# Optimization experiments

Measured on AMD Instinct MI355X. Metric: run time of the kernel, lower is better.

Reference implementation:

```python
import jax, jax.numpy as jnp
import numpy as np

HEADS = 8

def _grid_edges(H, W):
    # 4-neighbor grid adjacency, built at trace time (static), faithful to the torch double loop
    N = H * W
    idx = np.arange(N).reshape(H, W)
    e = np.zeros((N, N), np.float32)
    a, b = idx[1:, :].ravel(), idx[:-1, :].ravel()
    e[a, b] = 1.0; e[b, a] = 1.0
    a, b = idx[:, 1:].ravel(), idx[:, :-1].ravel()
    e[a, b] = 1.0; e[b, a] = 1.0
    return jnp.asarray(e)

def _layernorm(x, g, b, eps=1e-5):
    m = x.mean(-1, keepdims=True)
    v = x.var(-1, keepdims=True)
    return (x - m) / jnp.sqrt(v + eps) * g + b

def _gat(nodes, edges, W, b, rel):
    # nodes: [N,B,E]; W: [4,E,E] (q,k,v,out); rel: [HEADS]
    N, B, E = nodes.shape
    hd = E // HEADS
    q = (nodes @ W[0].T + b[0]).reshape(N, B, HEADS, hd)
    k = (nodes @ W[1].T + b[1]).reshape(N, B, HEADS, hd)
    v = (nodes @ W[2].T + b[2]).reshape(N, B, HEADS, hd)
    s = jnp.einsum('ibhd,jbhd->hbij', q, k) / float(np.sqrt(hd))
    s = s + edges[None, None] * rel[:, None, None, None]  # per-head edge relation bias
    a = jax.nn.softmax(s, axis=1)  # faithful to source: softmax over dim=1 (batch axis)
    o = jnp.einsum('hbij,jbhd->ibhd', a, v).reshape(N, B, E)
    return o @ W[3].T + b[3]

def _mha(q_in, kv_in, W, b):
    # standard nn.MultiheadAttention (eval, no dropout); seq-first [L,B,E]
    L, B, E = q_in.shape
    S = kv_in.shape[0]
    hd = E // HEADS
    q = (q_in @ W[0].T + b[0]).reshape(L, B, HEADS, hd)
    k = (kv_in @ W[1].T + b[1]).reshape(S, B, HEADS, hd)
    v = (kv_in @ W[2].T + b[2]).reshape(S, B, HEADS, hd)
    s = jnp.einsum('ibhd,jbhd->hbij', q, k) / float(np.sqrt(hd))
    a = jax.nn.softmax(s, axis=-1)
    o = jnp.einsum('hbij,jbhd->ibhd', a, v).reshape(L, B, E)
    return o @ W[3].T + b[3]

def reference(x, gat_W, gat_b, gat_rel, cross_W, cross_b, ln_g, ln_b):
    B, C, H, W = x.shape
    P = H // 4
    # global nodes: avg_pool2d(kernel=4) then flatten to [P*P, B, C]
    g = x.reshape(B, C, P, 4, P, 4).mean(axis=(3, 5))
    global_nodes = g.reshape(B, C, P * P).transpose(2, 0, 1)
    global_edges = jnp.ones((P * P, P * P), x.dtype)
    local_nodes = x.reshape(B, C, H * W).transpose(2, 0, 1)  # [HW,B,C]
    local_edges = _grid_edges(H, W)
    g_out = _gat(global_nodes, global_edges, gat_W[0], gat_b[0], gat_rel[0])
    g_out = _layernorm(g_out + global_nodes, ln_g[0], ln_b[0])
    l_out = _gat(local_nodes, local_edges, gat_W[1], gat_b[1], gat_rel[1])
    l_out = _layernorm(l_out + local_nodes, ln_g[1], ln_b[1])
    # nearest upsample x4 of global output back to HxW
    g_map = g_out.transpose(1, 2, 0).reshape(B, C, P, P)
    g_up = jnp.repeat(jnp.repeat(g_map, 4, axis=2), 4, axis=3)
    g_up = g_up.reshape(B, C, H * W).transpose(2, 0, 1)
    c_out = _mha(l_out, g_up, cross_W, cross_b)
    c_out = _layernorm(c_out + l_out, ln_g[2], ln_b[2])
    return c_out.transpose(1, 2, 0).reshape(B, C, H, W)

def setup_inputs() -> dict:
    key = jax.random.key(0)
    ks = jax.random.split(key, 6)
    B, C, H, W = 2, 256, 40, 40
    E = C
    sc = 0.02
    return {
        "x": jax.random.normal(ks[0], (B, C, H, W), jnp.float32),
        "gat_W": jax.random.normal(ks[1], (2, 4, E, E), jnp.float32) * sc,
        "gat_b": jax.random.normal(ks[2], (2, 4, E), jnp.float32) * sc,
        "gat_rel": jax.random.normal(ks[3], (2, HEADS), jnp.float32),
        "cross_W": jax.random.normal(ks[4], (4, E, E), jnp.float32) * sc,
        "cross_b": jax.random.normal(ks[5], (4, E), jnp.float32) * sc,
        "ln_g": jnp.ones((3, E), jnp.float32),
        "ln_b": jnp.zeros((3, E), jnp.float32),
    }
```

## Files before the change

### kernel.cpp

```cpp
#include <hip/hip_runtime.h>
#include <math.h>

#define NLOC 1600
#define NGLO 100

typedef unsigned short u16;
typedef short s16x8 __attribute__((ext_vector_type(8)));
typedef float f32x4 __attribute__((ext_vector_type(4)));

__device__ __forceinline__ short f2bf(float f) {
    unsigned u = __float_as_uint(f);
    u += 0x7fffu + ((u >> 16) & 1u);
    return (short)(u >> 16);
}
__device__ __forceinline__ float bf2f(u16 h) {
    return __uint_as_float(((unsigned)h) << 16);
}


__device__ __forceinline__ void gemm_tile(int lane, const u16* __restrict__ A,
                                          const u16* __restrict__ W,
                                          const float* __restrict__ bias,
                                          u16* __restrict__ C, int M, int m0, int n0) {
    int c = lane & 15, qd = lane >> 4;
    f32x4 acc[2][4] = {};
#pragma unroll 2
    for (int kc = 0; kc < 8; ++kc) {
        int ko = kc * 32 + qd * 8;
        s16x8 af[2], bf[4];
#pragma unroll
        for (int mi = 0; mi < 2; ++mi) {
            int row = m0 + mi * 16 + c;
            s16x8 zz = {};
            af[mi] = (row < M) ? *(const s16x8*)(A + (size_t)row * 256 + ko) : zz;
        }
#pragma unroll
        for (int ni = 0; ni < 4; ++ni)
            bf[ni] = *(const s16x8*)(W + (size_t)(n0 + ni * 16 + c) * 256 + ko);
#pragma unroll
        for (int mi = 0; mi < 2; ++mi)
#pragma unroll
            for (int ni = 0; ni < 4; ++ni)
                acc[mi][ni] = __builtin_amdgcn_mfma_f32_16x16x32_bf16(af[mi], bf[ni],
                                                                      acc[mi][ni], 0, 0, 0);
    }
#pragma unroll
    for (int mi = 0; mi < 2; ++mi)
#pragma unroll
        for (int r = 0; r < 4; ++r) {
            int row = m0 + mi * 16 + 4 * qd + r;
            if (row < M) {
#pragma unroll
                for (int ni = 0; ni < 4; ++ni) {
                    int col = n0 + ni * 16 + c;
                    C[(size_t)row * 256 + col] = (u16)f2bf(acc[mi][ni][r] + bias[col]);
                }
            }
        }
}

template <int MODE>
__device__ __forceinline__ void gemmln_block(int tid, const u16* __restrict__ A,
                                             const u16* __restrict__ W,
                                             const float* __restrict__ bias,
                                             const float* __restrict__ R,
                                             const float* __restrict__ g,
                                             const float* __restrict__ bb,
                                             float* fout, u16* bfout, float* dout,
                                             int M, int m0) {
    int w = tid >> 6, lane = tid & 63;
    int c = lane & 15, qd = lane >> 4;
    int n0 = w * 64;

    f32x4 acc[4] = {};
#pragma unroll 2
    for (int kc = 0; kc < 8; ++kc) {
        int ko = kc * 32 + qd * 8;
        int row = m0 + c;
        s16x8 zz = {};
        s16x8 af = (row < M) ? *(const s16x8*)(A + (size_t)row * 256 + ko) : zz;
#pragma unroll
        for (int ni = 0; ni < 4; ++ni) {
            s16x8 bf = *(const s16x8*)(W + (size_t)(n0 + ni * 16 + c) * 256 + ko);
            acc[ni] = __builtin_amdgcn_mfma_f32_16x16x32_bf16(af, bf, acc[ni], 0, 0, 0);
        }
    }

    __shared__ float ps1[4][16], ps2[4][16];
    float v[4][4];
#pragma unroll
    for (int r = 0; r < 4; ++r) {
        int row = m0 + 4 * qd + r;
        bool ok = (row < M);
        float s1 = 0.f, s2 = 0.f;
#pragma unroll
        for (int ni = 0; ni < 4; ++ni) {
            int col = n0 + ni * 16 + c;
            float val = acc[ni][r] + bias[col] + (ok ? R[(size_t)row * 256 + col] : 0.f);
            v[r][ni] = val;
            s1 += val; s2 += val * val;
        }
        s1 += __shfl_xor(s1, 1); s2 += __shfl_xor(s2, 1);
        s1 += __shfl_xor(s1, 2); s2 += __shfl_xor(s2, 2);
        s1 += __shfl_xor(s1, 4); s2 += __shfl_xor(s2, 4);
        s1 += __shfl_xor(s1, 8); s2 += __shfl_xor(s2, 8);
        if (c == 0) { ps1[w][4 * qd + r] = s1; ps2[w][4 * qd + r] = s2; }
    }
    __syncthreads();

    if (MODE == 0) {
#pragma unroll
        for (int r = 0; r < 4; ++r) {
            int lr = 4 * qd + r;
            int row = m0 + lr;
            if (row >= M) continue;
            float s1 = ps1[0][lr] + ps1[1][lr] + ps1[2][lr] + ps1[3][lr];
            float s2 = ps2[0][lr] + ps2[1][lr] + ps2[2][lr] + ps2[3][lr];
            float mean = s1 * (1.f / 256.f);
            float var  = s2 * (1.f / 256.f) - mean * mean;
            float rstd = rsqrtf(var + 1e-5f);
#pragma unroll
            for (int ni = 0; ni < 4; ++ni) {
                int col = n0 + ni * 16 + c;
                float y = (v[r][ni] - mean) * rstd * g[col] + bb[col];
                fout[(size_t)row * 256 + col] = y;
                bfout[(size_t)row * 256 + col] = (u16)f2bf(y);
            }
        }
    } else {
        __shared__ float ytile[2][8][256];
#pragma unroll
        for (int r = 0; r < 4; ++r) {
            int lr = 4 * qd + r;
            float s1 = ps1[0][lr] + ps1[1][lr] + ps1[2][lr] + ps1[3][lr];
            float s2 = ps2[0][lr] + ps2[1][lr] + ps2[2][lr] + ps2[3][lr];
            float mean = s1 * (1.f / 256.f);
            float var  = s2 * (1.f / 256.f) - mean * mean;
            float rstd = rsqrtf(var + 1e-5f);
#pragma unroll
            for (int ni = 0; ni < 4; ++ni) {
                int col = n0 + ni * 16 + c;
                ytile[lr & 1][lr >> 1][col] = (v[r][ni] - mean) * rstd * g[col] + bb[col];
            }
        }
        __syncthreads();
#pragma unroll
        for (int p = tid; p < 512; p += 256) {
            int b = p >> 8, col = p & 255;
            float4 y0, y1;
            y0.x = ytile[b][0][col]; y0.y = ytile[b][1][col];
            y0.z = ytile[b][2][col]; y0.w = ytile[b][3][col];
            y1.x = ytile[b][4][col]; y1.y = ytile[b][5][col];
            y1.z = ytile[b][6][col]; y1.w = ytile[b][7][col];
            size_t o = ((size_t)(b * 256 + col)) * 1600 + (m0 >> 1);
            *(float4*)(dout + o)     = y0;
            *(float4*)(dout + o + 4) = y1;
        }
    }
}

__global__ __launch_bounds__(256) void k_prep(const float* __restrict__ gw,
                                              const float* __restrict__ cw,
                                              u16* __restrict__ gwb,
                                              u16* __restrict__ cwb,
                                              const float* __restrict__ x,
                                              float* __restrict__ nodes,
                                              u16* __restrict__ nodesb,
                                              float* __restrict__ gn,
                                              u16* __restrict__ gnb) {
    int bx = blockIdx.x;
    if (bx < 768) {
        int t = bx * 256 + threadIdx.x;
        const float* src; u16* dst; int idx;
        if (t < 131072) { src = gw; dst = gwb; idx = t; }
        else            { src = cw; dst = cwb; idx = t - 131072; }
        float4 v = ((const float4*)src)[idx];
        ushort4 o;
        o.x = (u16)f2bf(v.x); o.y = (u16)f2bf(v.y);
        o.z = (u16)f2bf(v.z); o.w = (u16)f2bf(v.w);
        ((ushort4*)dst)[idx] = o;
        return;
    }
    int bid = bx - 768;
    if (bid < 3200) {
        int t = bid * 256 + threadIdx.x;
        int c = t & 255;
        int b = (t >> 8) & 1;
        int n = t >> 9;
        float v = x[((size_t)(b * 256 + c)) * 1600 + n];
        nodes[t] = v;
        nodesb[t] = (u16)f2bf(v);
    } else {
        int t = (bid - 3200) * 256 + threadIdx.x;
        int c = t & 255;
        int b = (t >> 8) & 1;
        int n = t >> 9;
        int p = n / 10, qq = n - p * 10;
        const float* xp = x + ((size_t)(b * 256 + c)) * 1600 + (p * 4) * 40 + qq * 4;
        float s = 0.f;
#pragma unroll
        for (int dy = 0; dy < 4; ++dy)
#pragma unroll
            for (int dx = 0; dx < 4; ++dx)
                s += xp[dy * 40 + dx];
        s *= (1.f / 16.f);
        gn[t] = s;
        gnb[t] = (u16)f2bf(s);
    }
}

__global__ __launch_bounds__(64) void k_qkv(const u16* __restrict__ nodesb,
                                            const u16* __restrict__ gnb,
                                            const u16* __restrict__ W1b,
                                            const u16* __restrict__ W0b,
                                            const float* __restrict__ b1,
                                            const float* __restrict__ b0,
                                            u16* __restrict__ qbuf,
                                            u16* __restrict__ gqb,
                                            float* __restrict__ sv1) {
    int lane = threadIdx.x;
    int bx = blockIdx.x, z = blockIdx.z;
    int n0 = blockIdx.y * 64;
    if (bx == 100 && blockIdx.y == 0 && z == 0) {
#pragma unroll
        for (int i = 0; i < 8; ++i) sv1[lane * 8 + i] = 0.f;
    }
    if (bx < 100)
        gemm_tile(lane, nodesb, W1b + (size_t)z * 65536, b1 + z * 256,
                  qbuf + (size_t)z * 819200, 3200, bx * 32, n0);
    else
        gemm_tile(lane, gnb, W0b + (size_t)z * 65536, b0 + z * 256,
                  gqb + (size_t)z * 51200, 200, (bx - 100) * 32, n0);
}

__device__ __forceinline__ void vtrans_block(const u16* __restrict__ src,
                                             u16* __restrict__ dst,
                                             int M, int Npad, int bxx, int byy,
                                             float* sum) {
    __shared__ u16 tile[32][33];
    int m0 = bxx * 32;
    int e0 = byy * 32;
    int tx = threadIdx.x & 31, ty = threadIdx.x >> 5;
#pragma unroll
    for (int k2 = 0; k2 < 4; ++k2) {
        int m = m0 + ty + k2 * 8;
        tile[ty + k2 * 8][tx] = (m < M) ? src[(size_t)m * 256 + e0 + tx] : (u16)0;
    }
    __syncthreads();
    int b = tx >> 4, nl = tx & 15;
    int n = (m0 >> 1) + nl;
    if (n < Npad) {
#pragma unroll
        for (int k2 = 0; k2 < 4; ++k2) {
            int e = e0 + ty + k2 * 8;
            dst[(size_t)(b * 256 + e) * Npad + n] = tile[2 * nl + b][ty + k2 * 8];
        }
    }
    if (threadIdx.x < 32) {
        float s = 0.f;
#pragma unroll
        for (int r = 0; r < 16; ++r) s += bf2f(tile[2 * r + 1][threadIdx.x]);
        atomicAdd(&sum[e0 + threadIdx.x], s);
    }
}

__global__ __launch_bounds__(256) void k_vtrans(const u16* __restrict__ vbuf,
                                                u16* __restrict__ vtb,
                                                const u16* __restrict__ gvb,
                                                u16* __restrict__ gvt,
                                                float* __restrict__ sv1l,
                                                float* __restrict__ sv1g) {
    int bx = blockIdx.x;
    if (bx < 100) vtrans_block(vbuf, vtb, 3200, 1600, bx, blockIdx.y, sv1l);
    else          vtrans_block(gvb, gvt, 200, 128, bx - 100, blockIdx.y, sv1g);
}

__global__ __launch_bounds__(256) void k_attn(
    const u16* __restrict__ qb, const u16* __restrict__ kb,
    const u16* __restrict__ vt, float* __restrict__ pO, float* __restrict__ pT,
    const u16* __restrict__ gqb, const u16* __restrict__ gkb,
    const u16* __restrict__ gvt, const float* __restrict__ sv1g,
    u16* __restrict__ gattb)
{
    __shared__ u16 ks[2][32][40];
    __shared__ u16 vs[2][32][40];
    __shared__ short At4[4][16][40];

    int tid = threadIdx.x;
    int w = tid >> 6, lane = tid & 63;
    int c = lane & 15, qd = lane >> 4;
    int bx = blockIdx.x;

    if (bx < 800) {
        int q4 = bx & 3;
        int hic = bx >> 2;
        int ic = hic % 25, h = hic / 25;
        int hb = h * 32;
        int i0 = ic * 64 + w * 16;
        int jb0 = q4 * 13, jbe = (jb0 + 13 < 50) ? jb0 + 13 : 50;

        const u16* qp = qb + ((size_t)(i0 + c) * 2) * 256 + hb + qd * 8;
        s16x8 qf0 = *(const s16x8*)qp;
        s16x8 qf1 = *(const s16x8*)(qp + 256);
#pragma unroll
        for (int z = 0; z < 8; ++z) qf0[z] ^= (short)0x8000;

        f32x4 o0[2] = {}, t1[2] = {};

        int srow = tid >> 2, part = tid & 3;
        int sjl = srow >> 1, sb = srow & 1;
        int vb_ = srow >> 5, vd = srow & 31;

        for (int jb = jb0; jb < jbe; ++jb) {
            int j0 = jb * 32;
            __syncthreads();
            {
                s16x8 kv = *(const s16x8*)(kb + (size_t)(j0 + sjl) * 512 + sb * 256 + hb + part * 8);
                *(s16x8*)&ks[sb][sjl][part * 8] = kv;
                s16x8 vv = *(const s16x8*)(vt + (size_t)(vb_ * 256 + hb + vd) * 1600 + j0 + part * 8);
                *(s16x8*)&vs[vb_][vd][part * 8] = vv;
            }
            __syncthreads();

            s16x8 kf00 = *(const s16x8*)&ks[0][c][qd * 8];
            s16x8 kf10 = *(const s16x8*)&ks[1][c][qd * 8];
            s16x8 kf01 = *(const s16x8*)&ks[0][16 + c][qd * 8];
            s16x8 kf11 = *(const s16x8*)&ks[1][16 + c][qd * 8];

            f32x4 z4 = {};
            f32x4 sd0 = __builtin_amdgcn_mfma_f32_16x16x32_bf16(qf0, kf00, z4, 0, 0, 0);
            sd0       = __builtin_amdgcn_mfma_f32_16x16x32_bf16(qf1, kf10, sd0, 0, 0, 0);
            f32x4 sd1 = __builtin_amdgcn_mfma_f32_16x16x32_bf16(qf0, kf01, z4, 0, 0, 0);
            sd1       = __builtin_amdgcn_mfma_f32_16x16x32_bf16(qf1, kf11, sd1, 0, 0, 0);
#pragma unroll
            for (int r = 0; r < 4; ++r) {
                float e0v = __expf(sd0[r] * 0.17677669529663687f);
                At4[w][4 * qd + r][c]      = f2bf(__builtin_amdgcn_rcpf(1.f + e0v));
                float e1v = __expf(sd1[r] * 0.17677669529663687f);
                At4[w][4 * qd + r][16 + c] = f2bf(__builtin_amdgcn_rcpf(1.f + e1v));
            }
            asm volatile("s_waitcnt lgkmcnt(0)" ::: "memory");
            s16x8 af = *(const s16x8*)&At4[w][c][qd * 8];

            s16x8 vf00 = *(const s16x8*)&vs[0][c][qd * 8];
            s16x8 vf01 = *(const s16x8*)&vs[0][16 + c][qd * 8];
            s16x8 vf10 = *(const s16x8*)&vs[1][c][qd * 8];
            s16x8 vf11 = *(const s16x8*)&vs[1][16 + c][qd * 8];

            o0[0] = __builtin_amdgcn_mfma_f32_16x16x32_bf16(af, vf00, o0[0], 0, 0, 0);
            o0[1] = __builtin_amdgcn_mfma_f32_16x16x32_bf16(af, vf01, o0[1], 0, 0, 0);
            t1[0] = __builtin_amdgcn_mfma_f32_16x16x32_bf16(af, vf10, t1[0], 0, 0, 0);
            t1[1] = __builtin_amdgcn_mfma_f32_16x16x32_bf16(af, vf11, t1[1], 0, 0, 0);
        }

        size_t base = (size_t)q4 * 409600;
#pragma unroll
        for (int dh = 0; dh < 2; ++dh)
#pragma unroll
            for (int r = 0; r < 4; ++r) {
                size_t idx = base + (size_t)(i0 + 4 * qd + r) * 256 + hb + dh * 16 + c;
                pO[idx] = o0[dh][r];
                pT[idx] = t1[dh][r];
            }
    } else {
        int idx = (bx - 800) * 4 + w;
        int h = idx / 7, it = idx % 7;
        int i0 = it * 16;
        int hb = h * 32;

        s16x8 qf0 = {}, qf1 = {};
        int i = i0 + c;
        if (i < NGLO) {
            const u16* qp = gqb + ((size_t)i * 2) * 256 + hb + qd * 8;
            qf0 = *(const s16x8*)qp;
            qf1 = *(const s16x8*)(qp + 256);
        }
#pragma unroll
        for (int z = 0; z < 8; ++z) qf0[z] ^= (short)0x8000;

        f32x4 o0[2] = {}, t1[2] = {};

        for (int j0 = 0; j0 < NGLO; j0 += 32) {
            s16x8 kf[2][2], vf[2][2];
#pragma unroll
            for (int b = 0; b < 2; ++b)
#pragma unroll
                for (int js = 0; js < 2; ++js) {
                    int j = j0 + js * 16 + c;
                    s16x8 kv = {};
                    if (j < NGLO) kv = *(const s16x8*)(gkb + ((size_t)j * 2 + b) * 256 + hb + qd * 8);
                    kf[b][js] = kv;
                }
#pragma unroll
            for (int b = 0; b < 2; ++b)
#pragma unroll
                for (int dh = 0; dh < 2; ++dh)
                    vf[b][dh] = *(const s16x8*)(gvt + (size_t)(b * 256 + hb + dh * 16 + c) * 128
                                                + j0 + qd * 8);

            f32x4 z4 = {};
            f32x4 sd0 = __builtin_amdgcn_mfma_f32_16x16x32_bf16(qf0, kf[0][0], z4, 0, 0, 0);
            sd0       = __builtin_amdgcn_mfma_f32_16x16x32_bf16(qf1, kf[1][0], sd0, 0, 0, 0);
            f32x4 sd1 = __builtin_amdgcn_mfma_f32_16x16x32_bf16(qf0, kf[0][1], z4, 0, 0, 0);
            sd1       = __builtin_amdgcn_mfma_f32_16x16x32_bf16(qf1, kf[1][1], sd1, 0, 0, 0);
#pragma unroll
            for (int r = 0; r < 4; ++r) {
                float e0v = __expf(sd0[r] * 0.17677669529663687f);
                At4[w][4 * qd + r][c]      = f2bf(__builtin_amdgcn_rcpf(1.f + e0v));
                float e1v = __expf(sd1[r] * 0.17677669529663687f);
                At4[w][4 * qd + r][16 + c] = f2bf(__builtin_amdgcn_rcpf(1.f + e1v));
            }
            asm volatile("s_waitcnt lgkmcnt(0)" ::: "memory");
            s16x8 af = *(const s16x8*)&At4[w][c][qd * 8];
            o0[0] = __builtin_amdgcn_mfma_f32_16x16x32_bf16(af, vf[0][0], o0[0], 0, 0, 0);
            o0[1] = __builtin_amdgcn_mfma_f32_16x16x32_bf16(af, vf[0][1], o0[1], 0, 0, 0);
            t1[0] = __builtin_amdgcn_mfma_f32_16x16x32_bf16(af, vf[1][0], t1[0], 0, 0, 0);
            t1[1] = __builtin_amdgcn_mfma_f32_16x16x32_bf16(af, vf[1][1], t1[1], 0, 0, 0);
        }

#pragma unroll
        for (int dh = 0; dh < 2; ++dh) {
            float sv = sv1g[hb + dh * 16 + c];
#pragma unroll
            for (int r = 0; r < 4; ++r) {
                int ii = i0 + 4 * qd + r;
                if (ii < NGLO) {
                    size_t o = ((size_t)ii * 2) * 256 + hb + dh * 16 + c;
                    gattb[o]       = (u16)f2bf(o0[dh][r]);
                    gattb[o + 256] = (u16)f2bf(sv - t1[dh][r]);
                }
            }
        }
    }
}

__global__ __launch_bounds__(256) void k_combine_gproj(
    const float* __restrict__ pO, const float* __restrict__ pT,
    const float* __restrict__ sv1l, u16* __restrict__ attb,
    const u16* __restrict__ gattb, const u16* __restrict__ W0p,
    const float* __restrict__ b0p, const float* __restrict__ gn,
    const float* __restrict__ ln_g, const float* __restrict__ ln_b,
    float* __restrict__ gout, u16* __restrict__ goutb)
{
    int bx = blockIdx.x;
    if (bx < 400) {
        int t4 = (bx * 256 + threadIdx.x) * 4;
        int e = t4 & 255;
        int i = t4 >> 8;
        float4 o  = *(const float4*)(pO + t4);
        float4 tt = *(const float4*)(pT + t4);
#pragma unroll
        for (int q = 1; q < 4; ++q) {
            float4 a = *(const float4*)(pO + t4 + q * 409600);
            float4 b = *(const float4*)(pT + t4 + q * 409600);
            o.x += a.x; o.y += a.y; o.z += a.z; o.w += a.w;
            tt.x += b.x; tt.y += b.y; tt.z += b.z; tt.w += b.w;
        }
        float4 sv = *(const float4*)(sv1l + e);
        ushort4 w0, w1;
        w0.x = (u16)f2bf(o.x); w0.y = (u16)f2bf(o.y);
        w0.z = (u16)f2bf(o.z); w0.w = (u16)f2bf(o.w);
        w1.x = (u16)f2bf(sv.x - tt.x); w1.y = (u16)f2bf(sv.y - tt.y);
        w1.z = (u16)f2bf(sv.z - tt.z); w1.w = (u16)f2bf(sv.w - tt.w);
        *(ushort4*)(attb + (size_t)i * 512 + e)       = w0;
        *(ushort4*)(attb + (size_t)i * 512 + 256 + e) = w1;
    } else {
        gemmln_block<0>(threadIdx.x, gattb, W0p, b0p, gn, ln_g, ln_b,
                        gout, goutb, (float*)0, 200, (bx - 400) * 16);
    }
}

__global__ __launch_bounds__(256) void k_lproj_ckcv(
    const u16* __restrict__ attb, const u16* __restrict__ W1p,
    const float* __restrict__ b1p, const float* __restrict__ nodes,
    const float* __restrict__ ln_g1, const float* __restrict__ ln_b1,
    float* __restrict__ lout, u16* __restrict__ loutb,
    const u16* __restrict__ goutb, const u16* __restrict__ wckv,
    const float* __restrict__ bckv, u16* __restrict__ ckb)
{
    int bx = blockIdx.x;
    if (bx < 200) {
        gemmln_block<0>(threadIdx.x, attb, W1p, b1p, nodes, ln_g1, ln_b1,
                        lout, loutb, (float*)0, 3200, bx * 16);
    } else {
        int w = threadIdx.x >> 6, lane = threadIdx.x & 63;
        int idx = (bx - 200) * 4 + w;
        int z = idx / 28, rem = idx % 28;
        int m0 = (rem >> 2) * 32, n0 = (rem & 3) * 64;
        gemm_tile(lane, goutb, wckv + (size_t)z * 65536, bckv + z * 256,
                  ckb + (size_t)z * 51200, 200, m0, n0);
    }
}

__global__ __launch_bounds__(256) void k_cq_vtrans(
    const u16* __restrict__ loutb, const u16* __restrict__ wcq,
    const float* __restrict__ bcq, u16* __restrict__ cqb,
    const u16* __restrict__ cvb, u16* __restrict__ cvt)
{
    int bx = blockIdx.x;
    if (bx < 100) {
        int w = threadIdx.x >> 6, lane = threadIdx.x & 63;
        int idx = bx * 4 + w;
        int m0 = (idx % 100) * 32, n0 = (idx / 100) * 64;
        gemm_tile(lane, loutb, wcq, bcq, cqb, 3200, m0, n0);
    } else {
        int bb = bx - 100;
        __shared__ u16 tile[32][33];
        int m0 = (bb & 7) * 32;
        int e0 = (bb >> 3) * 32;
        int tx = threadIdx.x & 31, ty = threadIdx.x >> 5;
#pragma unroll
        for (int k2 = 0; k2 < 4; ++k2) {
            int m = m0 + ty + k2 * 8;
            tile[ty + k2 * 8][tx] = (m < 200) ? cvb[(size_t)m * 256 + e0 + tx] : (u16)0;
        }
        __syncthreads();
        int b = tx >> 4, nl = tx & 15;
        int n = (m0 >> 1) + nl;
#pragma unroll
        for (int k2 = 0; k2 < 4; ++k2) {
            int e = e0 + ty + k2 * 8;
            cvt[(size_t)(b * 256 + e) * 128 + n] = tile[2 * nl + b][ty + k2 * 8];
        }
    }
}

__global__ __launch_bounds__(256) void k_cross(
    const u16* __restrict__ qb, const u16* __restrict__ kb,
    const u16* __restrict__ vt, u16* __restrict__ out)
{
    __shared__ short At[4][16][136];
    int w = threadIdx.x >> 6, lane = threadIdx.x & 63;
    int c  = lane & 15;
    int qd = lane >> 4;
    int idx = blockIdx.x * 4 + w;
    int it = idx % 100;
    int hb2 = idx / 100;
    int h = hb2 >> 1, b = hb2 & 1;
    int i0 = it * 16;
    int hb = h * 32;

    for (int z = lane; z < 16 * 24; z += 64)
        At[w][z / 24][112 + (z % 24)] = 0;

    const u16* qp = qb + ((size_t)(i0 + c) * 2 + b) * 256 + hb + qd * 8;
    s16x8 qf = *(const s16x8*)qp;

    f32x4 s[7];
#pragma unroll
    for (int jt = 0; jt < 7; ++jt) {
        int j = jt * 16 + c;
        s16x8 kf = {};
        if (j < NGLO) kf = *(const s16x8*)(kb + ((size_t)j * 2 + b) * 256 + hb + qd * 8);
        f32x4 z4 = {};
        s[jt] = __builtin_amdgcn_mfma_f32_16x16x32_bf16(qf, kf, z4, 0, 0, 0);
    }
    if (c >= 4) {
#pragma unroll
        for (int r = 0; r < 4; ++r) s[6][r] = -1e30f;
    }
#pragma unroll
    for (int jt = 0; jt < 7; ++jt)
#pragma unroll
        for (int r = 0; r < 4; ++r) s[jt][r] *= 0.17677669529663687f;

    float l[4];
#pragma unroll
    for (int r = 0; r < 4; ++r) {
        float mm = s[0][r];
#pragma unroll
        for (int jt = 1; jt < 7; ++jt) mm = fmaxf(mm, s[jt][r]);
        mm = fmaxf(mm, __shfl_xor(mm, 1));
        mm = fmaxf(mm, __shfl_xor(mm, 2));
        mm = fmaxf(mm, __shfl_xor(mm, 4));
        mm = fmaxf(mm, __shfl_xor(mm, 8));
        float ll = 0.f;
#pragma unroll
        for (int jt = 0; jt < 7; ++jt) {
            float p = __expf(s[jt][r] - mm);
            s[jt][r] = p;
            ll += p;
        }
        ll += __shfl_xor(ll, 1);
        ll += __shfl_xor(ll, 2);
        ll += __shfl_xor(ll, 4);
        ll += __shfl_xor(ll, 8);
        l[r] = ll;
    }
#pragma unroll
    for (int jt = 0; jt < 7; ++jt)
#pragma unroll
        for (int r = 0; r < 4; ++r)
            At[w][4 * qd + r][jt * 16 + c] = f2bf(s[jt][r]);
    asm volatile("s_waitcnt lgkmcnt(0)" ::: "memory");

    f32x4 o[2] = {};
#pragma unroll
    for (int kc = 0; kc < 4; ++kc) {
        s16x8 af = *(const s16x8*)&At[w][c][kc * 32 + qd * 8];
#pragma unroll
        for (int dh = 0; dh < 2; ++dh) {
            s16x8 vf = *(const s16x8*)(vt + (size_t)(b * 256 + hb + dh * 16 + c) * 128
                                       + kc * 32 + qd * 8);
            o[dh] = __builtin_amdgcn_mfma_f32_16x16x32_bf16(af, vf, o[dh], 0, 0, 0);
        }
    }
#pragma unroll
    for (int dh = 0; dh < 2; ++dh)
#pragma unroll
        for (int r = 0; r < 4; ++r) {
            int ii = i0 + 4 * qd + r;
            out[((size_t)ii * 2 + b) * 256 + hb + dh * 16 + c] = (u16)f2bf(o[dh][r] / l[r]);
        }
}

__global__ __launch_bounds__(256) void k_cproj(
    const u16* __restrict__ cattb, const u16* __restrict__ wcp,
    const float* __restrict__ bcp, const float* __restrict__ lout,
    const float* __restrict__ ln_g2, const float* __restrict__ ln_b2,
    float* __restrict__ dout)
{
    gemmln_block<1>(threadIdx.x, cattb, wcp, bcp, lout, ln_g2, ln_b2,
                    (float*)0, (u16*)0, dout, 3200, blockIdx.x * 16);
}

extern "C" void kernel_launch(void* const* d_in, const int* in_sizes, int n_in,
                              void* d_out, int out_size, void* d_ws, size_t ws_size,
                              hipStream_t stream) {
    const float* x        = (const float*)d_in[0];
    const float* gat_W    = (const float*)d_in[1];
    const float* gat_b    = (const float*)d_in[2];
    const float* cross_W  = (const float*)d_in[4];
    const float* cross_b  = (const float*)d_in[5];
    const float* ln_g     = (const float*)d_in[6];
    const float* ln_b     = (const float*)d_in[7];
    float* out = (float*)d_out;

    float* ws    = (float*)d_ws;
    float* nodes = ws;
    float* lout  = nodes + 819200;
    float* proj  = lout  + 819200;
    float* gn    = proj  + 819200;
    float* gprj  = gn    + 51200;
    float* gout  = gprj  + 51200;
    float* sv1l  = gout  + 51200;
    float* sv1g  = sv1l  + 256;
    float* pT    = sv1g  + 256;
    float* pO    = lout;
    u16* wgatb  = (u16*)(pT + 1638400);
    u16* wcrsb  = wgatb + 524288;
    u16* nodesb = wcrsb + 262144;
    u16* qbuf   = nodesb + 819200;
    u16* kbuf   = qbuf + 819200;
    u16* vbuf   = kbuf + 819200;
    u16* vtb    = vbuf + 819200;
    u16* attb   = vtb + 819200;
    u16* gnb    = attb + 819200;
    u16* gqb    = gnb + 51200;
    u16* gkb    = gqb + 51200;
    u16* gvb    = gkb + 51200;
    u16* gvt    = gvb + 51200;
    u16* gattb  = gvt + 65536;
    u16* goutb  = gattb + 51200;
    u16* ckb    = goutb + 51200;
    u16* cvb    = ckb + 51200;
    u16* cvt    = cvb + 51200;
    u16* loutb  = vbuf;
    u16* cqb    = attb;
    u16* cattb  = kbuf;

    const u16* W0b = wgatb;
    const u16* W1b = wgatb + 4 * 65536;
    const float* b0 = gat_b;
    const float* b1 = gat_b + 4 * 256;

    k_prep<<<4168, 256, 0, stream>>>(gat_W, cross_W, wgatb, wcrsb,
                                     x, nodes, nodesb, gn, gnb);
    k_qkv<<<dim3(107, 4, 3), 64, 0, stream>>>(nodesb, gnb, W1b, W0b, b1, b0,
                                              qbuf, gqb, sv1l);
    k_vtrans<<<dim3(108, 8), 256, 0, stream>>>(vbuf, vtb, gvb, gvt, sv1l, sv1g);
    k_attn<<<814, 256, 0, stream>>>(qbuf, kbuf, vtb, pO, pT,
                                    gqb, gkb, gvt, sv1g, gattb);
    k_combine_gproj<<<413, 256, 0, stream>>>(pO, pT, sv1l, attb,
                                             gattb, W0b + 3 * 65536, b0 + 768, gn,
                                             ln_g, ln_b, gout, goutb);
    k_lproj_ckcv<<<214, 256, 0, stream>>>(attb, W1b + 3 * 65536, b1 + 768, nodes,
                                          ln_g + 256, ln_b + 256, lout, loutb,
                                          goutb, wcrsb + 65536, cross_b + 256, ckb);
    k_cq_vtrans<<<164, 256, 0, stream>>>(loutb, wcrsb, cross_b, cqb, cvb, cvt);
    k_cross<<<400, 256, 0, stream>>>(cqb, ckb, cvt, cattb);
    k_cproj<<<200, 256, 0, stream>>>(cattb, wcrsb + 3 * 65536, cross_b + 768, lout,
                                     ln_g + 512, ln_b + 512, out);
}
```

Measured before the change: 167.0 us.

## Fuse all stages into one cooperative persistent kernel with grid syncs

Replaces the nine separate kernel launches with a single cooperative persistent kernel. Each stage loops over tasks and stages are separated by grid.sync(). The V transpose is folded into the QKV GEMM epilogue, which writes the transposed layout directly and accumulates the column sums atomically. The x-to-nodes conversion now goes through an LDS-tiled transpose. This removes launch gaps and the separate transpose passes, at the cost of grid-wide barrier overhead, occupancy limits from the shared smem footprint, and load imbalance across phases.

```diff
diff --git a/kernel.cpp b/kernel.cpp
--- a/kernel.cpp
+++ b/kernel.cpp
@@ -1,5 +1,8 @@
 #include <hip/hip_runtime.h>
+#include <hip/hip_cooperative_groups.h>
 #include <math.h>
+
+namespace cg = cooperative_groups;
 
 #define NLOC 1600
 #define NGLO 100
@@ -17,13 +20,22 @@
     return __uint_as_float(((unsigned)h) << 16);
 }
 
-
-__device__ __forceinline__ void gemm_tile(int lane, const u16* __restrict__ A,
+struct P {
+    const float *x, *gat_W, *gat_b, *cross_W, *cross_b, *ln_g, *ln_b;
+    float *out;
+    float *nodes, *gn, *gout, *lout, *sv1l, *sv1g, *pO, *pT;
+    u16 *wgatb, *wcrsb, *nodesb, *gnb, *qbuf, *kbuf, *vtb, *gqb, *gkb, *gvt,
+        *gattb, *goutb, *attb, *loutb, *ckb, *cvt, *cqb, *cattb;
+};
+
+__device__ __forceinline__ void gemm_core(int lane, const u16* __restrict__ A,
                                           const u16* __restrict__ W,
-                                          const float* __restrict__ bias,
-                                          u16* __restrict__ C, int M, int m0, int n0) {
+                                          int M, int m0, int n0, f32x4 acc[2][4]) {
     int c = lane & 15, qd = lane >> 4;
-    f32x4 acc[2][4] = {};
+#pragma unroll
+    for (int mi = 0; mi < 2; ++mi)
+#pragma unroll
+        for (int ni = 0; ni < 4; ++ni) acc[mi][ni] = (f32x4){0.f, 0.f, 0.f, 0.f};
 #pragma unroll 2
     for (int kc = 0; kc < 8; ++kc) {
         int ko = kc * 32 + qd * 8;
@@ -44,6 +56,12 @@
                 acc[mi][ni] = __builtin_amdgcn_mfma_f32_16x16x32_bf16(af[mi], bf[ni],
                                                                       acc[mi][ni], 0, 0, 0);
     }
+}
+
+__device__ __forceinline__ void ep_row(int lane, f32x4 acc[2][4],
+                                       const float* __restrict__ bias,
+                                       u16* __restrict__ C, int M, int m0, int n0) {
+    int c = lane & 15, qd = lane >> 4;
 #pragma unroll
     for (int mi = 0; mi < 2; ++mi)
 #pragma unroll
@@ -59,8 +77,38 @@
         }
 }
 
+__device__ __forceinline__ void ep_vt(int lane, f32x4 acc[2][4],
+                                      const float* __restrict__ bias,
+                                      u16* __restrict__ vt, int Npad,
+                                      int M, int m0, int n0, float* sum) {
+    int c = lane & 15, qd = lane >> 4;
+    float s[4] = {0.f, 0.f, 0.f, 0.f};
+#pragma unroll
+    for (int mi = 0; mi < 2; ++mi)
+#pragma unroll
+        for (int r = 0; r < 4; ++r) {
+            int row = m0 + mi * 16 + 4 * qd + r;
+            if (row < M) {
+                int n = row >> 1, b = row & 1;
+#pragma unroll
+                for (int ni = 0; ni < 4; ++ni) {
+                    int col = n0 + ni * 16 + c;
+                    float val = acc[mi][ni][r] + bias[col];
+                    vt[(size_t)(b * 256 + col) * Npad + n] = (u16)f2bf(val);
+                    if (b) s[ni] += val;
+                }
+            }
+        }
+    if (sum) {
+#pragma unroll
+        for (int ni = 0; ni < 4; ++ni)
+            atomicAdd(&sum[n0 + ni * 16 + c], s[ni]);
+    }
+}
+
 template <int MODE>
-__device__ __forceinline__ void gemmln_block(int tid, const u16* __restrict__ A,
+__device__ __forceinline__ void gemmln_block(int tid, unsigned char* smem,
+                                             const u16* __restrict__ A,
                                              const u16* __restrict__ W,
                                              const float* __restrict__ bias,
                                              const float* __restrict__ R,
@@ -71,6 +119,9 @@
     int w = tid >> 6, lane = tid & 63;
     int c = lane & 15, qd = lane >> 4;
     int n0 = w * 64;
+    float (*ps1)[16] = (float(*)[16])smem;
+    float (*ps2)[16] = (float(*)[16])(smem + 256);
+    float (*ytile)[8][256] = (float(*)[8][256])(smem + 512);
 
     f32x4 acc[4] = {};
 #pragma unroll 2
@@ -86,7 +137,6 @@
         }
     }
 
-    __shared__ float ps1[4][16], ps2[4][16];
     float v[4][4];
 #pragma unroll
     for (int r = 0; r < 4; ++r) {
@@ -128,7 +178,6 @@
             }
         }
     } else {
-        __shared__ float ytile[2][8][256];
 #pragma unroll
         for (int r = 0; r < 4; ++r) {
             int lr = 4 * qd + r;
@@ -145,8 +194,8 @@
         }
         __syncthreads();
 #pragma unroll
-        for (int p = tid; p < 512; p += 256) {
-            int b = p >> 8, col = p & 255;
+        for (int pp = tid; pp < 512; pp += 256) {
+            int b = pp >> 8, col = pp & 255;
             float4 y0, y1;
             y0.x = ytile[b][0][col]; y0.y = ytile[b][1][col];
             y0.z = ytile[b][2][col]; y0.w = ytile[b][3][col];
@@ -157,538 +206,457 @@
             *(float4*)(dout + o + 4) = y1;
         }
     }
-}
-
-__global__ __launch_bounds__(256) void k_prep(const float* __restrict__ gw,
-                                              const float* __restrict__ cw,
-                                              u16* __restrict__ gwb,
-                                              u16* __restrict__ cwb,
-                                              const float* __restrict__ x,
-                                              float* __restrict__ nodes,
-                                              u16* __restrict__ nodesb,
-                                              float* __restrict__ gn,
-                                              u16* __restrict__ gnb) {
-    int bx = blockIdx.x;
-    if (bx < 768) {
-        int t = bx * 256 + threadIdx.x;
-        const float* src; u16* dst; int idx;
-        if (t < 131072) { src = gw; dst = gwb; idx = t; }
-        else            { src = cw; dst = cwb; idx = t - 131072; }
-        float4 v = ((const float4*)src)[idx];
-        ushort4 o;
-        o.x = (u16)f2bf(v.x); o.y = (u16)f2bf(v.y);
-        o.z = (u16)f2bf(v.z); o.w = (u16)f2bf(v.w);
-        ((ushort4*)dst)[idx] = o;
-        return;
-    }
-    int bid = bx - 768;
-    if (bid < 3200) {
-        int t = bid * 256 + threadIdx.x;
-        int c = t & 255;
-        int b = (t >> 8) & 1;
-        int n = t >> 9;
-        float v = x[((size_t)(b * 256 + c)) * 1600 + n];
-        nodes[t] = v;
-        nodesb[t] = (u16)f2bf(v);
-    } else {
-        int t = (bid - 3200) * 256 + threadIdx.x;
-        int c = t & 255;
-        int b = (t >> 8) & 1;
-        int n = t >> 9;
-        int p = n / 10, qq = n - p * 10;
-        const float* xp = x + ((size_t)(b * 256 + c)) * 1600 + (p * 4) * 40 + qq * 4;
-        float s = 0.f;
-#pragma unroll
-        for (int dy = 0; dy < 4; ++dy)
-#pragma unroll
-            for (int dx = 0; dx < 4; ++dx)
-                s += xp[dy * 40 + dx];
-        s *= (1.f / 16.f);
-        gn[t] = s;
-        gnb[t] = (u16)f2bf(s);
-    }
-}
-
-__global__ __launch_bounds__(64) void k_qkv(const u16* __restrict__ nodesb,
-                                            const u16* __restrict__ gnb,
-                                            const u16* __restrict__ W1b,
-                                            const u16* __restrict__ W0b,
-                                            const float* __restrict__ b1,
-                                            const float* __restrict__ b0,
-                                            u16* __restrict__ qbuf,
-                                            u16* __restrict__ gqb,
-                                            float* __restrict__ sv1) {
-    int lane = threadIdx.x;
-    int bx = blockIdx.x, z = blockIdx.z;
-    int n0 = blockIdx.y * 64;
-    if (bx == 100 && blockIdx.y == 0 && z == 0) {
-#pragma unroll
-        for (int i = 0; i < 8; ++i) sv1[lane * 8 + i] = 0.f;
-    }
-    if (bx < 100)
-        gemm_tile(lane, nodesb, W1b + (size_t)z * 65536, b1 + z * 256,
-                  qbuf + (size_t)z * 819200, 3200, bx * 32, n0);
-    else
-        gemm_tile(lane, gnb, W0b + (size_t)z * 65536, b0 + z * 256,
-                  gqb + (size_t)z * 51200, 200, (bx - 100) * 32, n0);
-}
-
-__device__ __forceinline__ void vtrans_block(const u16* __restrict__ src,
-                                             u16* __restrict__ dst,
-                                             int M, int Npad, int bxx, int byy,
-                                             float* sum) {
-    __shared__ u16 tile[32][33];
-    int m0 = bxx * 32;
-    int e0 = byy * 32;
-    int tx = threadIdx.x & 31, ty = threadIdx.x >> 5;
-#pragma unroll
-    for (int k2 = 0; k2 < 4; ++k2) {
-        int m = m0 + ty + k2 * 8;
-        tile[ty + k2 * 8][tx] = (m < M) ? src[(size_t)m * 256 + e0 + tx] : (u16)0;
-    }
     __syncthreads();
-    int b = tx >> 4, nl = tx & 15;
-    int n = (m0 >> 1) + nl;
-    if (n < Npad) {
-#pragma unroll
-        for (int k2 = 0; k2 < 4; ++k2) {
-            int e = e0 + ty + k2 * 8;
-            dst[(size_t)(b * 256 + e) * Npad + n] = tile[2 * nl + b][ty + k2 * 8];
-        }
-    }
-    if (threadIdx.x < 32) {
-        float s = 0.f;
-#pragma unroll
-        for (int r = 0; r < 16; ++r) s += bf2f(tile[2 * r + 1][threadIdx.x]);
-        atomicAdd(&sum[e0 + threadIdx.x], s);
-    }
-}
-
-__global__ __launch_bounds__(256) void k_vtrans(const u16* __restrict__ vbuf,
-                                                u16* __restrict__ vtb,
-                                                const u16* __restrict__ gvb,
-                                                u16* __restrict__ gvt,
-                                                float* __restrict__ sv1l,
-                                                float* __restrict__ sv1g) {
-    int bx = blockIdx.x;
-    if (bx < 100) vtrans_block(vbuf, vtb, 3200, 1600, bx, blockIdx.y, sv1l);
-    else          vtrans_block(gvb, gvt, 200, 128, bx - 100, blockIdx.y, sv1g);
-}
-
-__global__ __launch_bounds__(256) void k_attn(
-    const u16* __restrict__ qb, const u16* __restrict__ kb,
-    const u16* __restrict__ vt, float* __restrict__ pO, float* __restrict__ pT,
-    const u16* __restrict__ gqb, const u16* __restrict__ gkb,
-    const u16* __restrict__ gvt, const float* __restrict__ sv1g,
-    u16* __restrict__ gattb)
-{
-    __shared__ u16 ks[2][32][40];
-    __shared__ u16 vs[2][32][40];
-    __shared__ short At4[4][16][40];
-
-    int tid = threadIdx.x;
-    int w = tid >> 6, lane = tid & 63;
-    int c = lane & 15, qd = lane >> 4;
-    int bx = blockIdx.x;
-
-    if (bx < 800) {
-        int q4 = bx & 3;
-        int hic = bx >> 2;
-        int ic = hic % 25, h = hic / 25;
-        int hb = h * 32;
-        int i0 = ic * 64 + w * 16;
-        int jb0 = q4 * 13, jbe = (jb0 + 13 < 50) ? jb0 + 13 : 50;
-
-        const u16* qp = qb + ((size_t)(i0 + c) * 2) * 256 + hb + qd * 8;
-        s16x8 qf0 = *(const s16x8*)qp;
-        s16x8 qf1 = *(const s16x8*)(qp + 256);
-#pragma unroll
-        for (int z = 0; z < 8; ++z) qf0[z] ^= (short)0x8000;
-
-        f32x4 o0[2] = {}, t1[2] = {};
-
-        int srow = tid >> 2, part = tid & 3;
-        int sjl = srow >> 1, sb = srow & 1;
-        int vb_ = srow >> 5, vd = srow & 31;
-
-        for (int jb = jb0; jb < jbe; ++jb) {
-            int j0 = jb * 32;
+}
+
+__global__ __launch_bounds__(256, 4) void mega(P p) {
+    cg::grid_group grid = cg::this_grid();
+    __shared__ __align__(16) unsigned char smem[17536];
+    const int tid = threadIdx.x;
+    const int w = tid >> 6, lane = tid & 63;
+    const int c = lane & 15, qd = lane >> 4;
+    const int nB = gridDim.x;
+
+    for (int task = blockIdx.x; task < 1771; task += nB) {
+        if (task < 768) {
+            int t = task * 256 + tid;
+            const float* src; u16* dst; int idx;
+            if (t < 131072) { src = p.gat_W; dst = p.wgatb; idx = t; }
+            else            { src = p.cross_W; dst = p.wcrsb; idx = t - 131072; }
+            float4 v = ((const float4*)src)[idx];
+            ushort4 o;
+            o.x = (u16)f2bf(v.x); o.y = (u16)f2bf(v.y);
+            o.z = (u16)f2bf(v.z); o.w = (u16)f2bf(v.w);
+            ((ushort4*)dst)[idx] = o;
+        } else if (task < 1568) {
+            float (*tile)[33] = (float(*)[33])smem;
+            int tt = task - 768;
+            int cb = tt / 100, rem = tt - cb * 100;
+            int nb = rem >> 1, b = rem & 1;
+            int c0 = cb * 32, n0t = nb * 32;
+            int tx = tid & 31, ty = tid >> 5;
+#pragma unroll
+            for (int k2 = 0; k2 < 4; ++k2) {
+                int cc = c0 + ty + k2 * 8;
+                tile[ty + k2 * 8][tx] = p.x[((size_t)(b * 256 + cc)) * 1600 + n0t + tx];
+            }
             __syncthreads();
-            {
-                s16x8 kv = *(const s16x8*)(kb + (size_t)(j0 + sjl) * 512 + sb * 256 + hb + part * 8);
-                *(s16x8*)&ks[sb][sjl][part * 8] = kv;
-                s16x8 vv = *(const s16x8*)(vt + (size_t)(vb_ * 256 + hb + vd) * 1600 + j0 + part * 8);
-                *(s16x8*)&vs[vb_][vd][part * 8] = vv;
+#pragma unroll
+            for (int k2 = 0; k2 < 4; ++k2) {
+                int n = n0t + ty + k2 * 8;
+                float val = tile[tx][ty + k2 * 8];
+                size_t o = ((size_t)(n * 2 + b)) * 256 + c0 + tx;
+                p.nodes[o] = val;
+                p.nodesb[o] = (u16)f2bf(val);
             }
             __syncthreads();
-
-            s16x8 kf00 = *(const s16x8*)&ks[0][c][qd * 8];
-            s16x8 kf10 = *(const s16x8*)&ks[1][c][qd * 8];
-            s16x8 kf01 = *(const s16x8*)&ks[0][16 + c][qd * 8];
-            s16x8 kf11 = *(const s16x8*)&ks[1][16 + c][qd * 8];
-
-            f32x4 z4 = {};
-            f32x4 sd0 = __builtin_amdgcn_mfma_f32_16x16x32_bf16(qf0, kf00, z4, 0, 0, 0);
-            sd0       = __builtin_amdgcn_mfma_f32_16x16x32_bf16(qf1, kf10, sd0, 0, 0, 0);
-            f32x4 sd1 = __builtin_amdgcn_mfma_f32_16x16x32_bf16(qf0, kf01, z4, 0, 0, 0);
-            sd1       = __builtin_amdgcn_mfma_f32_16x16x32_bf16(qf1, kf11, sd1, 0, 0, 0);
+        } else if (task < 1768) {
+            int pt = task - 1568;
+            int b = pt & 1, n = pt >> 1;
+            int cc = tid;
+            int pr = n / 10, qqc = n - pr * 10;
+            const float* xp = p.x + ((size_t)(b * 256 + cc)) * 1600 + (pr * 4) * 40 + qqc * 4;
+            float s = 0.f;
+#pragma unroll
+            for (int dy = 0; dy < 4; ++dy)
+#pragma unroll
+                for (int dx = 0; dx < 4; ++dx)
+                    s += xp[dy * 40 + dx];
+            s *= (1.f / 16.f);
+            size_t t = (size_t)pt * 256 + cc;
+            p.gn[t] = s;
+            p.gnb[t] = (u16)f2bf(s);
+        } else if (task == 1768) {
+            p.sv1l[tid] = 0.f;
+            p.sv1l[tid + 256] = 0.f;
+        } else if (task == 1769) {
+            for (int e2 = tid; e2 < 512; e2 += 256)
+                for (int n = 100; n < 128; ++n) p.gvt[(size_t)e2 * 128 + n] = 0;
+        } else {
+            for (int e2 = tid; e2 < 512; e2 += 256)
+                for (int n = 100; n < 128; ++n) p.cvt[(size_t)e2 * 128 + n] = 0;
+        }
+    }
+    grid.sync();
+
+    for (int wt = blockIdx.x * 4 + w; wt < 1284; wt += nB * 4) {
+        int z = wt / 428, rem = wt - z * 428;
+        int y = rem / 107, bx = rem - y * 107;
+        int n0 = y * 64;
+        f32x4 acc[2][4];
+        if (bx < 100) {
+            int m0 = bx * 32;
+            gemm_core(lane, p.nodesb, p.wgatb + (size_t)(4 + z) * 65536, 3200, m0, n0, acc);
+            const float* bias = p.gat_b + (4 + z) * 256;
+            if (z == 0)      ep_row(lane, acc, bias, p.qbuf, 3200, m0, n0);
+            else if (z == 1) ep_row(lane, acc, bias, p.kbuf, 3200, m0, n0);
+            else             ep_vt(lane, acc, bias, p.vtb, 1600, 3200, m0, n0, p.sv1l);
+        } else {
+            int m0 = (bx - 100) * 32;
+            gemm_core(lane, p.gnb, p.wgatb + (size_t)z * 65536, 200, m0, n0, acc);
+            const float* bias = p.gat_b + z * 256;
+            if (z == 0)      ep_row(lane, acc, bias, p.gqb, 200, m0, n0);
+            else if (z == 1) ep_row(lane, acc, bias, p.gkb, 200, m0, n0);
+            else             ep_vt(lane, acc, bias, p.gvt, 128, 200, m0, n0, p.sv1g);
+        }
+    }
+    grid.sync();
+
+    {
+        u16 (*ks)[32][40] = (u16(*)[32][40])smem;
+        u16 (*vs)[32][40] = (u16(*)[32][40])(smem + 5120);
+        short (*At4)[16][40] = (short(*)[16][40])(smem + 10240);
+        for (int task = blockIdx.x; task < 814; task += nB) {
+            if (task < 800) {
+                int q4 = task & 3;
+                int hic = task >> 2;
+                int ic = hic % 25, h = hic / 25;
+                int hb = h * 32;
+                int i0 = ic * 64 + w * 16;
+                int jb0 = q4 * 13, jbe = (jb0 + 13 < 50) ? jb0 + 13 : 50;
+
+                const u16* qp = p.qbuf + ((size_t)(i0 + c) * 2) * 256 + hb + qd * 8;
+                s16x8 qf0 = *(const s16x8*)qp;
+                s16x8 qf1 = *(const s16x8*)(qp + 256);
+#pragma unroll
+                for (int z = 0; z < 8; ++z) qf0[z] ^= (short)0x8000;
+
+                f32x4 o0[2] = {}, t1[2] = {};
+                int srow = tid >> 2, part = tid & 3;
+                int sjl = srow >> 1, sb = srow & 1;
+                int vb_ = srow >> 5, vd = srow & 31;
+
+                for (int jb = jb0; jb < jbe; ++jb) {
+                    int j0 = jb * 32;
+                    __syncthreads();
+                    {
+                        s16x8 kv = *(const s16x8*)(p.kbuf + (size_t)(j0 + sjl) * 512 + sb * 256 + hb + part * 8);
+                        *(s16x8*)&ks[sb][sjl][part * 8] = kv;
+                        s16x8 vv = *(const s16x8*)(p.vtb + (size_t)(vb_ * 256 + hb + vd) * 1600 + j0 + part * 8);
+                        *(s16x8*)&vs[vb_][vd][part * 8] = vv;
+                    }
+                    __syncthreads();
+
+                    s16x8 kf00 = *(const s16x8*)&ks[0][c][qd * 8];
+                    s16x8 kf10 = *(const s16x8*)&ks[1][c][qd * 8];
+                    s16x8 kf01 = *(const s16x8*)&ks[0][16 + c][qd * 8];
+                    s16x8 kf11 = *(const s16x8*)&ks[1][16 + c][qd * 8];
+
+                    f32x4 z4 = {};
+                    f32x4 sd0 = __builtin_amdgcn_mfma_f32_16x16x32_bf16(qf0, kf00, z4, 0, 0, 0);
+                    sd0       = __builtin_amdgcn_mfma_f32_16x16x32_bf16(qf1, kf10, sd0, 0, 0, 0);
+                    f32x4 sd1 = __builtin_amdgcn_mfma_f32_16x16x32_bf16(qf0, kf01, z4, 0, 0, 0);
+                    sd1       = __builtin_amdgcn_mfma_f32_16x16x32_bf16(qf1, kf11, sd1, 0, 0, 0);
+#pragma unroll
+                    for (int r = 0; r < 4; ++r) {
+                        float e0v = __expf(sd0[r] * 0.17677669529663687f);
+                        At4[w][4 * qd + r][c]      = f2bf(__builtin_amdgcn_rcpf(1.f + e0v));
+                        float e1v = __expf(sd1[r] * 0.17677669529663687f);
+                        At4[w][4 * qd + r][16 + c] = f2bf(__builtin_amdgcn_rcpf(1.f + e1v));
+                    }
+                    asm volatile("s_waitcnt lgkmcnt(0)" ::: "memory");
+                    s16x8 af = *(const s16x8*)&At4[w][c][qd * 8];
+
+                    s16x8 vf00 = *(const s16x8*)&vs[0][c][qd * 8];
+                    s16x8 vf01 = *(const s16x8*)&vs[0][16 + c][qd * 8];
+                    s16x8 vf10 = *(const s16x8*)&vs[1][c][qd * 8];
+                    s16x8 vf11 = *(const s16x8*)&vs[1][16 + c][qd * 8];
+
+                    o0[0] = __builtin_amdgcn_mfma_f32_16x16x32_bf16(af, vf00, o0[0], 0, 0, 0);
+                    o0[1] = __builtin_amdgcn_mfma_f32_16x16x32_bf16(af, vf01, o0[1], 0, 0, 0);
+                    t1[0] = __builtin_amdgcn_mfma_f32_16x16x32_bf16(af, vf10, t1[0], 0, 0, 0);
+                    t1[1] = __builtin_amdgcn_mfma_f32_16x16x32_bf16(af, vf11, t1[1], 0, 0, 0);
+                }
+
+                size_t base = (size_t)q4 * 409600;
+#pragma unroll
+                for (int dh = 0; dh < 2; ++dh)
+#pragma unroll
+                    for (int r = 0; r < 4; ++r) {
+                        size_t idx = base + (size_t)(i0 + 4 * qd + r) * 256 + hb + dh * 16 + c;
+                        p.pO[idx] = o0[dh][r];
+                        p.pT[idx] = t1[dh][r];
+                    }
+                __syncthreads();
+            } else {
+                int idx = (task - 800) * 4 + w;
+                int h = idx / 7, it = idx % 7;
+                int i0 = it * 16;
+                int hb = h * 32;
+
+                s16x8 qf0 = {}, qf1 = {};
+                int i = i0 + c;
+                if (i < NGLO) {
+                    const u16* qp = p.gqb + ((size_t)i * 2) * 256 + hb + qd * 8;
+                    qf0 = *(const s16x8*)qp;
+                    qf1 = *(const s16x8*)(qp + 256);
+                }
+#pragma unroll
+                for (int z = 0; z < 8; ++z) qf0[z] ^= (short)0x8000;
+
+                f32x4 o0[2] = {}, t1[2] = {};
+                for (int j0 = 0; j0 < NGLO; j0 += 32) {
+                    s16x8 kf[2][2], vf[2][2];
+#pragma unroll
+                    for (int b = 0; b < 2; ++b)
+#pragma unroll
+                        for (int js = 0; js < 2; ++js) {
+                            int j = j0 + js * 16 + c;
+                            s16x8 kv = {};
+                            if (j < NGLO) kv = *(const s16x8*)(p.gkb + ((size_t)j * 2 + b) * 256 + hb + qd * 8);
+                            kf[b][js] = kv;
+                        }
+#pragma unroll
+                    for (int b = 0; b < 2; ++b)
+#pragma unroll
+                        for (int dh = 0; dh < 2; ++dh)
+                            vf[b][dh] = *(const s16x8*)(p.gvt + (size_t)(b * 256 + hb + dh * 16 + c) * 128
+                                                        + j0 + qd * 8);
+
+                    f32x4 z4 = {};
+                    f32x4 sd0 = __builtin_amdgcn_mfma_f32_16x16x32_bf16(qf0, kf[0][0], z4, 0, 0, 0);
+                    sd0       = __builtin_amdgcn_mfma_f32_16x16x32_bf16(qf1, kf[1][0], sd0, 0, 0, 0);
+                    f32x4 sd1 = __builtin_amdgcn_mfma_f32_16x16x32_bf16(qf0, kf[0][1], z4, 0, 0, 0);
+                    sd1       = __builtin_amdgcn_mfma_f32_16x16x32_bf16(qf1, kf[1][1], sd1, 0, 0, 0);
+#pragma unroll
+                    for (int r = 0; r < 4; ++r) {
+                        float e0v = __expf(sd0[r] * 0.17677669529663687f);
+                        At4[w][4 * qd + r][c]      = f2bf(__builtin_amdgcn_rcpf(1.f + e0v));
+                        float e1v = __expf(sd1[r] * 0.17677669529663687f);
+                        At4[w][4 * qd + r][16 + c] = f2bf(__builtin_amdgcn_rcpf(1.f + e1v));
+                    }
+                    asm volatile("s_waitcnt lgkmcnt(0)" ::: "memory");
+                    s16x8 af = *(const s16x8*)&At4[w][c][qd * 8];
+                    o0[0] = __builtin_amdgcn_mfma_f32_16x16x32_bf16(af, vf[0][0], o0[0], 0, 0, 0);
+                    o0[1] = __builtin_amdgcn_mfma_f32_16x16x32_bf16(af, vf[0][1], o0[1], 0, 0, 0);
+                    t1[0] = __builtin_amdgcn_mfma_f32_16x16x32_bf16(af, vf[1][0], t1[0], 0, 0, 0);
+                    t1[1] = __builtin_amdgcn_mfma_f32_16x16x32_bf16(af, vf[1][1], t1[1], 0, 0, 0);
+                }
+#pragma unroll
+                for (int dh = 0; dh < 2; ++dh) {
+                    float sv = p.sv1g[hb + dh * 16 + c];
+#pragma unroll
+                    for (int r = 0; r < 4; ++r) {
+                        int ii = i0 + 4 * qd + r;
+                        if (ii < NGLO) {
+                            size_t o = ((size_t)ii * 2) * 256 + hb + dh * 16 + c;
+                            p.gattb[o]       = (u16)f2bf(o0[dh][r]);
+                            p.gattb[o + 256] = (u16)f2bf(sv - t1[dh][r]);
+                        }
+                    }
+                }
+                __syncthreads();
+            }
+        }
+    }
+    grid.sync();
+
+    for (int task = blockIdx.x; task < 413; task += nB) {
+        if (task < 400) {
+            int t4 = (task * 256 + tid) * 4;
+            int e = t4 & 255;
+            int i = t4 >> 8;
+            float4 o  = *(const float4*)(p.pO + t4);
+            float4 tt = *(const float4*)(p.pT + t4);
+#pragma unroll
+            for (int q = 1; q < 4; ++q) {
+                float4 a = *(const float4*)(p.pO + t4 + q * 409600);
+                float4 b = *(const float4*)(p.pT + t4 + q * 409600);
+                o.x += a.x; o.y += a.y; o.z += a.z; o.w += a.w;
+                tt.x += b.x; tt.y += b.y; tt.z += b.z; tt.w += b.w;
+            }
+            float4 sv = *(const float4*)(p.sv1l + e);
+            ushort4 w0, w1;
+            w0.x = (u16)f2bf(o.x); w0.y = (u16)f2bf(o.y);
+            w0.z = (u16)f2bf(o.z); w0.w = (u16)f2bf(o.w);
+            w1.x = (u16)f2bf(sv.x - tt.x); w1.y = (u16)f2bf(sv.y - tt.y);
+            w1.z = (u16)f2bf(sv.z - tt.z); w1.w = (u16)f2bf(sv.w - tt.w);
+            *(ushort4*)(p.attb + (size_t)i * 512 + e)       = w0;
+            *(ushort4*)(p.attb + (size_t)i * 512 + 256 + e) = w1;
+        } else {
+            gemmln_block<0>(tid, smem, p.gattb, p.wgatb + 3 * 65536, p.gat_b + 768,
+                            p.gn, p.ln_g, p.ln_b, p.gout, p.goutb, (float*)0,
+                            200, (task - 400) * 16);
+        }
+    }
+    grid.sync();
+
+    for (int task = blockIdx.x; task < 214; task += nB) {
+        if (task < 200) {
+            gemmln_block<0>(tid, smem, p.attb, p.wgatb + 7 * 65536, p.gat_b + 1792,
+                            p.nodes, p.ln_g + 256, p.ln_b + 256, p.lout, p.loutb,
+                            (float*)0, 3200, task * 16);
+        } else {
+            int idx = (task - 200) * 4 + w;
+            if (idx < 56) {
+                int z = idx / 28, rem = idx % 28;
+                int m0 = (rem >> 2) * 32, n0 = (rem & 3) * 64;
+                f32x4 acc[2][4];
+                gemm_core(lane, p.goutb, p.wcrsb + (size_t)(1 + z) * 65536, 200, m0, n0, acc);
+                const float* bias = p.cross_b + (1 + z) * 256;
+                if (z == 0) ep_row(lane, acc, bias, p.ckb, 200, m0, n0);
+                else        ep_vt(lane, acc, bias, p.cvt, 128, 200, m0, n0, (float*)0);
+            }
+        }
+    }
+    grid.sync();
+
+    for (int wt = blockIdx.x * 4 + w; wt < 400; wt += nB * 4) {
+        int m0 = (wt % 100) * 32, n0 = (wt / 100) * 64;
+        f32x4 acc[2][4];
+        gemm_core(lane, p.loutb, p.wcrsb, 3200, m0, n0, acc);
+        ep_row(lane, acc, p.cross_b, p.cqb, 3200, m0, n0);
+    }
+    grid.sync();
+
+    {
+        short (*Atc)[16][136] = (short(*)[16][136])smem;
+        for (int task = blockIdx.x; task < 400; task += nB) {
+            int idx = task * 4 + w;
+            int it = idx % 100;
+            int hb2 = idx / 100;
+            int h = hb2 >> 1, b = hb2 & 1;
+            int i0 = it * 16;
+            int hb = h * 32;
+
+            for (int z = lane; z < 16 * 24; z += 64)
+                Atc[w][z / 24][112 + (z % 24)] = 0;
+
+            const u16* qp = p.cqb + ((size_t)(i0 + c) * 2 + b) * 256 + hb + qd * 8;
+            s16x8 qf = *(const s16x8*)qp;
+
+            f32x4 s[7];
+#pragma unroll
+            for (int jt = 0; jt < 7; ++jt) {
+                int j = jt * 16 + c;
+                s16x8 kf = {};
+                if (j < NGLO) kf = *(const s16x8*)(p.ckb + ((size_t)j * 2 + b) * 256 + hb + qd * 8);
+                f32x4 z4 = {};
+                s[jt] = __builtin_amdgcn_mfma_f32_16x16x32_bf16(qf, kf, z4, 0, 0, 0);
+            }
+            if (c >= 4) {
+#pragma unroll
+                for (int r = 0; r < 4; ++r) s[6][r] = -1e30f;
+            }
+#pragma unroll
+            for (int jt = 0; jt < 7; ++jt)
+#pragma unroll
+                for (int r = 0; r < 4; ++r) s[jt][r] *= 0.17677669529663687f;
+
+            float l[4];
 #pragma unroll
             for (int r = 0; r < 4; ++r) {
-                float e0v = __expf(sd0[r] * 0.17677669529663687f);
-                At4[w][4 * qd + r][c]      = f2bf(__builtin_amdgcn_rcpf(1.f + e0v));
-                float e1v = __expf(sd1[r] * 0.17677669529663687f);
-                At4[w][4 * qd + r][16 + c] = f2bf(__builtin_amdgcn_rcpf(1.f + e1v));
-            }
+                float mm = s[0][r];
+#pragma unroll
+                for (int jt = 1; jt < 7; ++jt) mm = fmaxf(mm, s[jt][r]);
+                mm = fmaxf(mm, __shfl_xor(mm, 1));
+                mm = fmaxf(mm, __shfl_xor(mm, 2));
+                mm = fmaxf(mm, __shfl_xor(mm, 4));
+                mm = fmaxf(mm, __shfl_xor(mm, 8));
+                float ll = 0.f;
+#pragma unroll
+                for (int jt = 0; jt < 7; ++jt) {
+                    float pv = __expf(s[jt][r] - mm);
+                    s[jt][r] = pv;
+                    ll += pv;
+                }
+                ll += __shfl_xor(ll, 1);
+                ll += __shfl_xor(ll, 2);
+                ll += __shfl_xor(ll, 4);
+                ll += __shfl_xor(ll, 8);
+                l[r] = ll;
+            }
+#pragma unroll
+            for (int jt = 0; jt < 7; ++jt)
+#pragma unroll
+                for (int r = 0; r < 4; ++r)
+                    Atc[w][4 * qd + r][jt * 16 + c] = f2bf(s[jt][r]);
             asm volatile("s_waitcnt lgkmcnt(0)" ::: "memory");
-            s16x8 af = *(const s16x8*)&At4[w][c][qd * 8];
-
-            s16x8 vf00 = *(const s16x8*)&vs[0][c][qd * 8];
-            s16x8 vf01 = *(const s16x8*)&vs[0][16 + c][qd * 8];
-            s16x8 vf10 = *(const s16x8*)&vs[1][c][qd * 8];
-            s16x8 vf11 = *(const s16x8*)&vs[1][16 + c][qd * 8];
-
-            o0[0] = __builtin_amdgcn_mfma_f32_16x16x32_bf16(af, vf00, o0[0], 0, 0, 0);
-            o0[1] = __builtin_amdgcn_mfma_f32_16x16x32_bf16(af, vf01, o0[1], 0, 0, 0);
-            t1[0] = __builtin_amdgcn_mfma_f32_16x16x32_bf16(af, vf10, t1[0], 0, 0, 0);
-            t1[1] = __builtin_amdgcn_mfma_f32_16x16x32_bf16(af, vf11, t1[1], 0, 0, 0);
-        }
-
-        size_t base = (size_t)q4 * 409600;
-#pragma unroll
-        for (int dh = 0; dh < 2; ++dh)
-#pragma unroll
-            for (int r = 0; r < 4; ++r) {
-                size_t idx = base + (size_t)(i0 + 4 * qd + r) * 256 + hb + dh * 16 + c;
-                pO[idx] = o0[dh][r];
-                pT[idx] = t1[dh][r];
-            }
-    } else {
-        int idx = (bx - 800) * 4 + w;
-        int h = idx / 7, it = idx % 7;
-        int i0 = it * 16;
-        int hb = h * 32;
-
-        s16x8 qf0 = {}, qf1 = {};
-        int i = i0 + c;
-        if (i < NGLO) {
-            const u16* qp = gqb + ((size_t)i * 2) * 256 + hb + qd * 8;
-            qf0 = *(const s16x8*)qp;
-            qf1 = *(const s16x8*)(qp + 256);
-        }
-#pragma unroll
-        for (int z = 0; z < 8; ++z) qf0[z] ^= (short)0x8000;
-
-        f32x4 o0[2] = {}, t1[2] = {};
-
-        for (int j0 = 0; j0 < NGLO; j0 += 32) {
-            s16x8 kf[2][2], vf[2][2];
-#pragma unroll
-            for (int b = 0; b < 2; ++b)
-#pragma unroll
-                for (int js = 0; js < 2; ++js) {
-                    int j = j0 + js * 16 + c;
-                    s16x8 kv = {};
-                    if (j < NGLO) kv = *(const s16x8*)(gkb + ((size_t)j * 2 + b) * 256 + hb + qd * 8);
-                    kf[b][js] = kv;
-                }
-#pragma unroll
-            for (int b = 0; b < 2; ++b)
-#pragma unroll
-                for (int dh = 0; dh < 2; ++dh)
-                    vf[b][dh] = *(const s16x8*)(gvt + (size_t)(b * 256 + hb + dh * 16 + c) * 128
-                                                + j0 + qd * 8);
-
-            f32x4 z4 = {};
-            f32x4 sd0 = __builtin_amdgcn_mfma_f32_16x16x32_bf16(qf0, kf[0][0], z4, 0, 0, 0);
-            sd0       = __builtin_amdgcn_mfma_f32_16x16x32_bf16(qf1, kf[1][0], sd0, 0, 0, 0);
-            f32x4 sd1 = __builtin_amdgcn_mfma_f32_16x16x32_bf16(qf0, kf[0][1], z4, 0, 0, 0);
-            sd1       = __builtin_amdgcn_mfma_f32_16x16x32_bf16(qf1, kf[1][1], sd1, 0, 0, 0);
-#pragma unroll
-            for (int r = 0; r < 4; ++r) {
-                float e0v = __expf(sd0[r] * 0.17677669529663687f);
-                At4[w][4 * qd + r][c]      = f2bf(__builtin_amdgcn_rcpf(1.f + e0v));
-                float e1v = __expf(sd1[r] * 0.17677669529663687f);
-                At4[w][4 * qd + r][16 + c] = f2bf(__builtin_amdgcn_rcpf(1.f + e1v));
-            }
-            asm volatile("s_waitcnt lgkmcnt(0)" ::: "memory");
-            s16x8 af = *(const s16x8*)&At4[w][c][qd * 8];
-            o0[0] = __builtin_amdgcn_mfma_f32_16x16x32_bf16(af, vf[0][0], o0[0], 0, 0, 0);
-            o0[1] = __builtin_amdgcn_mfma_f32_16x16x32_bf16(af, vf[0][1], o0[1], 0, 0, 0);
-            t1[0] = __builtin_amdgcn_mfma_f32_16x16x32_bf16(af, vf[1][0], t1[0], 0, 0, 0);
-            t1[1] = __builtin_amdgcn_mfma_f32_16x16x32_bf16(af, vf[1][1], t1[1], 0, 0, 0);
-        }
-
-#pragma unroll
-        for (int dh = 0; dh < 2; ++dh) {
-            float sv = sv1g[hb + dh * 16 + c];
-#pragma unroll
-            for (int r = 0; r < 4; ++r) {
-                int ii = i0 + 4 * qd + r;
-                if (ii < NGLO) {
-                    size_t o = ((size_t)ii * 2) * 256 + hb + dh * 16 + c;
-                    gattb[o]       = (u16)f2bf(o0[dh][r]);
-                    gattb[o + 256] = (u16)f2bf(sv - t1[dh][r]);
-                }
-            }
-        }
-    }
-}
-
-__global__ __launch_bounds__(256) void k_combine_gproj(
-    const float* __restrict__ pO, const float* __restrict__ pT,
-    const float* __restrict__ sv1l, u16* __restrict__ attb,
-    const u16* __restrict__ gattb, const u16* __restrict__ W0p,
-    const float* __restrict__ b0p, const float* __restrict__ gn,
-    const float* __restrict__ ln_g, const float* __restrict__ ln_b,
-    float* __restrict__ gout, u16* __restrict__ goutb)
-{
-    int bx = blockIdx.x;
-    if (bx < 400) {
-        int t4 = (bx * 256 + threadIdx.x) * 4;
-        int e = t4 & 255;
-        int i = t4 >> 8;
-        float4 o  = *(const float4*)(pO + t4);
-        float4 tt = *(const float4*)(pT + t4);
-#pragma unroll
-        for (int q = 1; q < 4; ++q) {
-            float4 a = *(const float4*)(pO + t4 + q * 409600);
-            float4 b = *(const float4*)(pT + t4 + q * 409600);
-            o.x += a.x; o.y += a.y; o.z += a.z; o.w += a.w;
-            tt.x += b.x; tt.y += b.y; tt.z += b.z; tt.w += b.w;
-        }
-        float4 sv = *(const float4*)(sv1l + e);
-        ushort4 w0, w1;
-        w0.x = (u16)f2bf(o.x); w0.y = (u16)f2bf(o.y);
-        w0.z = (u16)f2bf(o.z); w0.w = (u16)f2bf(o.w);
-        w1.x = (u16)f2bf(sv.x - tt.x); w1.y = (u16)f2bf(sv.y - tt.y);
-        w1.z = (u16)f2bf(sv.z - tt.z); w1.w = (u16)f2bf(sv.w - tt.w);
-        *(ushort4*)(attb + (size_t)i * 512 + e)       = w0;
-        *(ushort4*)(attb + (size_t)i * 512 + 256 + e) = w1;
-    } else {
-        gemmln_block<0>(threadIdx.x, gattb, W0p, b0p, gn, ln_g, ln_b,
-                        gout, goutb, (float*)0, 200, (bx - 400) * 16);
-    }
-}
-
-__global__ __launch_bounds__(256) void k_lproj_ckcv(
-    const u16* __restrict__ attb, const u16* __restrict__ W1p,
-    const float* __restrict__ b1p, const float* __restrict__ nodes,
-    const float* __restrict__ ln_g1, const float* __restrict__ ln_b1,
-    float* __restrict__ lout, u16* __restrict__ loutb,
-    const u16* __restrict__ goutb, const u16* __restrict__ wckv,
-    const float* __restrict__ bckv, u16* __restrict__ ckb)
-{
-    int bx = blockIdx.x;
-    if (bx < 200) {
-        gemmln_block<0>(threadIdx.x, attb, W1p, b1p, nodes, ln_g1, ln_b1,
-                        lout, loutb, (float*)0, 3200, bx * 16);
-    } else {
-        int w = threadIdx.x >> 6, lane = threadIdx.x & 63;
-        int idx = (bx - 200) * 4 + w;
-        int z = idx / 28, rem = idx % 28;
-        int m0 = (rem >> 2) * 32, n0 = (rem & 3) * 64;
-        gemm_tile(lane, goutb, wckv + (size_t)z * 65536, bckv + z * 256,
-                  ckb + (size_t)z * 51200, 200, m0, n0);
-    }
-}
-
-__global__ __launch_bounds__(256) void k_cq_vtrans(
-    const u16* __restrict__ loutb, const u16* __restrict__ wcq,
-    const float* __restrict__ bcq, u16* __restrict__ cqb,
-    const u16* __restrict__ cvb, u16* __restrict__ cvt)
-{
-    int bx = blockIdx.x;
-    if (bx < 100) {
-        int w = threadIdx.x >> 6, lane = threadIdx.x & 63;
-        int idx = bx * 4 + w;
-        int m0 = (idx % 100) * 32, n0 = (idx / 100) * 64;
-        gemm_tile(lane, loutb, wcq, bcq, cqb, 3200, m0, n0);
-    } else {
-        int bb = bx - 100;
-        __shared__ u16 tile[32][33];
-        int m0 = (bb & 7) * 32;
-        int e0 = (bb >> 3) * 32;
-        int tx = threadIdx.x & 31, ty = threadIdx.x >> 5;
-#pragma unroll
-        for (int k2 = 0; k2 < 4; ++k2) {
-            int m = m0 + ty + k2 * 8;
-            tile[ty + k2 * 8][tx] = (m < 200) ? cvb[(size_t)m * 256 + e0 + tx] : (u16)0;
-        }
-        __syncthreads();
-        int b = tx >> 4, nl = tx & 15;
-        int n = (m0 >> 1) + nl;
-#pragma unroll
-        for (int k2 = 0; k2 < 4; ++k2) {
-            int e = e0 + ty + k2 * 8;
-            cvt[(size_t)(b * 256 + e) * 128 + n] = tile[2 * nl + b][ty + k2 * 8];
-        }
-    }
-}
-
-__global__ __launch_bounds__(256) void k_cross(
-    const u16* __restrict__ qb, const u16* __restrict__ kb,
-    const u16* __restrict__ vt, u16* __restrict__ out)
-{
-    __shared__ short At[4][16][136];
-    int w = threadIdx.x >> 6, lane = threadIdx.x & 63;
-    int c  = lane & 15;
-    int qd = lane >> 4;
-    int idx = blockIdx.x * 4 + w;
-    int it = idx % 100;
-    int hb2 = idx / 100;
-    int h = hb2 >> 1, b = hb2 & 1;
-    int i0 = it * 16;
-    int hb = h * 32;
-
-    for (int z = lane; z < 16 * 24; z += 64)
-        At[w][z / 24][112 + (z % 24)] = 0;
-
-    const u16* qp = qb + ((size_t)(i0 + c) * 2 + b) * 256 + hb + qd * 8;
-    s16x8 qf = *(const s16x8*)qp;
-
-    f32x4 s[7];
-#pragma unroll
-    for (int jt = 0; jt < 7; ++jt) {
-        int j = jt * 16 + c;
-        s16x8 kf = {};
-        if (j < NGLO) kf = *(const s16x8*)(kb + ((size_t)j * 2 + b) * 256 + hb + qd * 8);
-        f32x4 z4 = {};
-        s[jt] = __builtin_amdgcn_mfma_f32_16x16x32_bf16(qf, kf, z4, 0, 0, 0);
-    }
-    if (c >= 4) {
-#pragma unroll
-        for (int r = 0; r < 4; ++r) s[6][r] = -1e30f;
-    }
-#pragma unroll
-    for (int jt = 0; jt < 7; ++jt)
-#pragma unroll
-        for (int r = 0; r < 4; ++r) s[jt][r] *= 0.17677669529663687f;
-
-    float l[4];
-#pragma unroll
-    for (int r = 0; r < 4; ++r) {
-        float mm = s[0][r];
-#pragma unroll
-        for (int jt = 1; jt < 7; ++jt) mm = fmaxf(mm, s[jt][r]);
-        mm = fmaxf(mm, __shfl_xor(mm, 1));
-        mm = fmaxf(mm, __shfl_xor(mm, 2));
-        mm = fmaxf(mm, __shfl_xor(mm, 4));
-        mm = fmaxf(mm, __shfl_xor(mm, 8));
-        float ll = 0.f;
-#pragma unroll
-        for (int jt = 0; jt < 7; ++jt) {
-            float p = __expf(s[jt][r] - mm);
-            s[jt][r] = p;
-            ll += p;
-        }
-        ll += __shfl_xor(ll, 1);
-        ll += __shfl_xor(ll, 2);
-        ll += __shfl_xor(ll, 4);
-        ll += __shfl_xor(ll, 8);
-        l[r] = ll;
-    }
-#pragma unroll
-    for (int jt = 0; jt < 7; ++jt)
-#pragma unroll
-        for (int r = 0; r < 4; ++r)
-            At[w][4 * qd + r][jt * 16 + c] = f2bf(s[jt][r]);
-    asm volatile("s_waitcnt lgkmcnt(0)" ::: "memory");
-
-    f32x4 o[2] = {};
-#pragma unroll
-    for (int kc = 0; kc < 4; ++kc) {
-        s16x8 af = *(const s16x8*)&At[w][c][kc * 32 + qd * 8];
-#pragma unroll
-        for (int dh = 0; dh < 2; ++dh) {
-            s16x8 vf = *(const s16x8*)(vt + (size_t)(b * 256 + hb + dh * 16 + c) * 128
-                                       + kc * 32 + qd * 8);
-            o[dh] = __builtin_amdgcn_mfma_f32_16x16x32_bf16(af, vf, o[dh], 0, 0, 0);
-        }
-    }
-#pragma unroll
-    for (int dh = 0; dh < 2; ++dh)
-#pragma unroll
-        for (int r = 0; r < 4; ++r) {
-            int ii = i0 + 4 * qd + r;
-            out[((size_t)ii * 2 + b) * 256 + hb + dh * 16 + c] = (u16)f2bf(o[dh][r] / l[r]);
-        }
-}
-
-__global__ __launch_bounds__(256) void k_cproj(
-    const u16* __restrict__ cattb, const u16* __restrict__ wcp,
-    const float* __restrict__ bcp, const float* __restrict__ lout,
-    const float* __restrict__ ln_g2, const float* __restrict__ ln_b2,
-    float* __restrict__ dout)
-{
-    gemmln_block<1>(threadIdx.x, cattb, wcp, bcp, lout, ln_g2, ln_b2,
-                    (float*)0, (u16*)0, dout, 3200, blockIdx.x * 16);
+
+            f32x4 o[2] = {};
+#pragma unroll
+            for (int kc = 0; kc < 4; ++kc) {
+                s16x8 af = *(const s16x8*)&Atc[w][c][kc * 32 + qd * 8];
+#pragma unroll
+                for (int dh = 0; dh < 2; ++dh) {
+                    s16x8 vf = *(const s16x8*)(p.cvt + (size_t)(b * 256 + hb + dh * 16 + c) * 128
+                                               + kc * 32 + qd * 8);
+                    o[dh] = __builtin_amdgcn_mfma_f32_16x16x32_bf16(af, vf, o[dh], 0, 0, 0);
+                }
+            }
+#pragma unroll
+            for (int dh = 0; dh < 2; ++dh)
+#pragma unroll
+                for (int r = 0; r < 4; ++r) {
+                    int ii = i0 + 4 * qd + r;
+                    p.cattb[((size_t)ii * 2 + b) * 256 + hb + dh * 16 + c] = (u16)f2bf(o[dh][r] / l[r]);
+                }
+        }
+    }
+    grid.sync();
+
+    for (int task = blockIdx.x; task < 200; task += nB) {
+        gemmln_block<1>(tid, smem, p.cattb, p.wcrsb + 3 * 65536, p.cross_b + 768,
+                        p.lout, p.ln_g + 512, p.ln_b + 512,
+                        (float*)0, (u16*)0, p.out, 3200, task * 16);
+    }
 }
 
 extern "C" void kernel_launch(void* const* d_in, const int* in_sizes, int n_in,
                               void* d_out, int out_size, void* d_ws, size_t ws_size,
                               hipStream_t stream) {
-    const float* x        = (const float*)d_in[0];
-    const float* gat_W    = (const float*)d_in[1];
-    const float* gat_b    = (const float*)d_in[2];
-    const float* cross_W  = (const float*)d_in[4];
-    const float* cross_b  = (const float*)d_in[5];
-    const float* ln_g     = (const float*)d_in[6];
-    const float* ln_b     = (const float*)d_in[7];
-    float* out = (float*)d_out;
-
-    float* ws    = (float*)d_ws;
-    float* nodes = ws;
-    float* lout  = nodes + 819200;
-    float* proj  = lout  + 819200;
-    float* gn    = proj  + 819200;
-    float* gprj  = gn    + 51200;
-    float* gout  = gprj  + 51200;
-    float* sv1l  = gout  + 51200;
-    float* sv1g  = sv1l  + 256;
-    float* pT    = sv1g  + 256;
-    float* pO    = lout;
-    u16* wgatb  = (u16*)(pT + 1638400);
-    u16* wcrsb  = wgatb + 524288;
-    u16* nodesb = wcrsb + 262144;
-    u16* qbuf   = nodesb + 819200;
-    u16* kbuf   = qbuf + 819200;
-    u16* vbuf   = kbuf + 819200;
-    u16* vtb    = vbuf + 819200;
-    u16* attb   = vtb + 819200;
-    u16* gnb    = attb + 819200;
-    u16* gqb    = gnb + 51200;
-    u16* gkb    = gqb + 51200;
-    u16* gvb    = gkb + 51200;
-    u16* gvt    = gvb + 51200;
-    u16* gattb  = gvt + 65536;
-    u16* goutb  = gattb + 51200;
-    u16* ckb    = goutb + 51200;
-    u16* cvb    = ckb + 51200;
-    u16* cvt    = cvb + 51200;
-    u16* loutb  = vbuf;
-    u16* cqb    = attb;
-    u16* cattb  = kbuf;
-
-    const u16* W0b = wgatb;
-    const u16* W1b = wgatb + 4 * 65536;
-    const float* b0 = gat_b;
-    const float* b1 = gat_b + 4 * 256;
-
-    k_prep<<<4168, 256, 0, stream>>>(gat_W, cross_W, wgatb, wcrsb,
-                                     x, nodes, nodesb, gn, gnb);
-    k_qkv<<<dim3(107, 4, 3), 64, 0, stream>>>(nodesb, gnb, W1b, W0b, b1, b0,
-                                              qbuf, gqb, sv1l);
-    k_vtrans<<<dim3(108, 8), 256, 0, stream>>>(vbuf, vtb, gvb, gvt, sv1l, sv1g);
-    k_attn<<<814, 256, 0, stream>>>(qbuf, kbuf, vtb, pO, pT,
-                                    gqb, gkb, gvt, sv1g, gattb);
-    k_combine_gproj<<<413, 256, 0, stream>>>(pO, pT, sv1l, attb,
-                                             gattb, W0b + 3 * 65536, b0 + 768, gn,
-                                             ln_g, ln_b, gout, goutb);
-    k_lproj_ckcv<<<214, 256, 0, stream>>>(attb, W1b + 3 * 65536, b1 + 768, nodes,
-                                          ln_g + 256, ln_b + 256, lout, loutb,
-                                          goutb, wcrsb + 65536, cross_b + 256, ckb);
-    k_cq_vtrans<<<164, 256, 0, stream>>>(loutb, wcrsb, cross_b, cqb, cvb, cvt);
-    k_cross<<<400, 256, 0, stream>>>(cqb, ckb, cvt, cattb);
-    k_cproj<<<200, 256, 0, stream>>>(cattb, wcrsb + 3 * 65536, cross_b + 768, lout,
-                                     ln_g + 512, ln_b + 512, out);
-}
+    float* ws = (float*)d_ws;
+
+    P p;
+    p.x       = (const float*)d_in[0];
+    p.gat_W   = (const float*)d_in[1];
+    p.gat_b   = (const float*)d_in[2];
+    p.cross_W = (const float*)d_in[4];
+    p.cross_b = (const float*)d_in[5];
+    p.ln_g    = (const float*)d_in[6];
+    p.ln_b    = (const float*)d_in[7];
+    p.out     = (float*)d_out;
+
+    p.nodes = ws;
+    p.gn    = p.nodes + 819200;
+    p.gout  = p.gn + 51200;
+    p.lout  = p.gout + 51200;
+    p.sv1l  = p.lout + 819200;
+    p.sv1g  = p.sv1l + 256;
+    p.pO    = p.sv1g + 256;
+    p.pT    = p.pO + 1638400;
+
+    u16* ub = (u16*)(p.pT + 1638400);
+    p.wgatb  = ub;                 ub += 524288;
+    p.wcrsb  = ub;                 ub += 262144;
+    p.nodesb = ub;                 ub += 819200;
+    p.gnb    = ub;                 ub += 51200;
+    p.qbuf   = ub;                 ub += 819200;
+    p.kbuf   = ub;                 ub += 819200;
+    p.vtb    = ub;                 ub += 819200;
+    p.gqb    = ub;                 ub += 51200;
+    p.gkb    = ub;                 ub += 51200;
+    p.gvt    = ub;                 ub += 65536;
+    p.gattb  = ub;                 ub += 51200;
+    p.goutb  = ub;                 ub += 51200;
+    p.attb   = ub;                 ub += 819200;
+    p.loutb  = ub;                 ub += 819200;
+    p.ckb    = ub;                 ub += 51200;
+    p.cvt    = ub;                 ub += 65536;
+    p.cqb    = ub;                 ub += 819200;
+    p.cattb  = ub;                 ub += 819200;
+
+    int nbPerCU = 0;
+    hipOccupancyMaxActiveBlocksPerMultiprocessor(&nbPerCU, mega, 256, 0);
+    if (nbPerCU < 1) nbPerCU = 1;
+    int dev = 0;
+    hipGetDevice(&dev);
+    int ncu = 0;
+    hipDeviceGetAttribute(&ncu, hipDeviceAttributeMultiprocessorCount, dev);
+    if (ncu < 1) ncu = 256;
+    int gridN = nbPerCU * ncu;
+    if (gridN > 1024) gridN = 1024;
+
+    void* args[] = {&p};
+    hipLaunchCooperativeKernel(mega, dim3(gridN), dim3(256), args, 0, stream);
+}
```

Result: slower. 608.9 us (+264.7%).
